# Optimization experiments

Measured on AMD Instinct MI355X. Metric: run time of the kernel, lower is better.

## Reference

```python
import jax, jax.numpy as jnp
import numpy as np

EMBED_SIZE = 1024
HEADS = 16
HEAD_DIM = EMBED_SIZE // HEADS  # 64


def setup_inputs() -> dict:
    key = jax.random.key(0)
    k_x, k_q, k_k, k_v, k_o, k_b = jax.random.split(key, 6)
    B, S = 32, 8192  # S divisible by HEADS
    x = jax.random.normal(k_x, (B, S, HEAD_DIM), dtype=jnp.float32)
    # torch.nn.Linear weights are [out, in]; scale ~ 1/sqrt(fan_in)
    s_h = 1.0 / np.sqrt(HEAD_DIM)
    s_e = 1.0 / np.sqrt(EMBED_SIZE)
    Wq = jax.random.uniform(k_q, (HEAD_DIM, HEAD_DIM), jnp.float32, -s_h, s_h)
    Wk = jax.random.uniform(k_k, (HEAD_DIM, HEAD_DIM), jnp.float32, -s_h, s_h)
    Wv = jax.random.uniform(k_v, (HEAD_DIM, HEAD_DIM), jnp.float32, -s_h, s_h)
    Wo = jax.random.uniform(k_o, (EMBED_SIZE, EMBED_SIZE), jnp.float32, -s_e, s_e)
    bo = jax.random.uniform(k_b, (EMBED_SIZE,), jnp.float32, -s_e, s_e)
    return {"x": x, "Wq": Wq, "Wk": Wk, "Wv": Wv, "Wo": Wo, "bo": bo}


def reference(x, Wq, Wk, Wv, Wo, bo):
    B = x.shape[0]
    # Q/K/V projections: Linear(head_dim, head_dim), bias=False -> x @ W.T
    Q = (x @ Wq.T).reshape(B, -1, HEADS, HEAD_DIM)  # [B, G, H, D], G = S/H
    K = (x @ Wk.T).reshape(B, -1, HEADS, HEAD_DIM)
    V = (x @ Wv.T).reshape(B, -1, HEADS, HEAD_DIM)
    # energy = Q @ K^T over last two dims -> [B, G, H, H]
    energy = jnp.einsum('bghd,bgkd->bghk', Q, K)
    attn = jax.nn.softmax(energy / jnp.sqrt(jnp.float32(EMBED_SIZE)), axis=3)
    out = jnp.einsum('bghk,bgkd->bghd', attn, V)      # [B, G, H, D]
    out = out.transpose(0, 2, 1, 3).reshape(B, -1, EMBED_SIZE)  # [B, S/H, E]
    return out @ Wo.T + bo
```

## Files before the change

### kernel.cpp

```cpp
#include <hip/hip_runtime.h>
#include <hip/hip_bf16.h>
#include <stdint.h>

#define TOKS   262144
#define NGRP   16384
#define EMB    1024
#define HD     64

using bf16x8 = __attribute__((ext_vector_type(8))) short;
using f32x4  = __attribute__((ext_vector_type(4))) float;

__device__ __forceinline__ unsigned pack2(float a, float b) {
    union { __hip_bfloat162 h; unsigned u; } cvt;
    cvt.h = __float22bfloat162_rn(make_float2(a, b));
    return cvt.u;
}
__device__ __forceinline__ bf16x8 cvt8(float4 v0, float4 v1) {
    uint4 u;
    u.x = pack2(v0.x, v0.y);
    u.y = pack2(v0.z, v0.w);
    u.z = pack2(v1.x, v1.y);
    u.w = pack2(v1.z, v1.w);
    return __builtin_bit_cast(bf16x8, u);
}
__device__ __forceinline__ void gload_lds16(const unsigned short* g, unsigned short* l) {
    __builtin_amdgcn_global_load_lds(
        (const __attribute__((address_space(1))) void*)g,
        (__attribute__((address_space(3))) void*)l,
        16, 0, 0);
}

__global__ __launch_bounds__(256) void k_cvt(const float* __restrict__ wo,
                                             const float* __restrict__ wq,
                                             const float* __restrict__ wk,
                                             const float* __restrict__ wv,
                                             unsigned short* __restrict__ wob,
                                             unsigned short* __restrict__ wqkvb) {
    int bid = blockIdx.x;
    if (bid < 512) {
        int tid = bid * 256 + threadIdx.x;
        int c   = tid >> 12;
        int nb  = (tid >> 6) & 63;
        int l   = tid & 63;
        int n   = nb * 16 + (l & 15);
        int k   = c * 32 + (l >> 4) * 8;
        const float* src = wo + (size_t)n * 1024 + k;
        float4 v0 = *(const float4*)(src);
        float4 v1 = *(const float4*)(src + 4);
        *(bf16x8*)(wob + (size_t)tid * 8) = cvt8(v0, v1);
    } else {
        int b = bid - 512;
        int m = b >> 2;
        const float* src = (m == 0) ? wq : ((m == 1) ? wk : wv);
        int idx = ((b & 3) * 256 + threadIdx.x) * 4;
        float4 v = *(const float4*)(src + idx);
        uint2 p;
        p.x = pack2(v.x, v.y);
        p.y = pack2(v.z, v.w);
        *(uint2*)(wqkvb + m * 4096 + idx) = p;
    }
}

#define SCL 0.0450842200278f

__global__ __launch_bounds__(256) void k_fused(const float* __restrict__ x,
                                               const unsigned short* __restrict__ wqkv,
                                               unsigned short* __restrict__ out2) {
    __shared__ __align__(16) unsigned short qkls[4][2][2][16 * 72];
    int t = threadIdx.x;
    int w = t >> 6, l = t & 63;
    int c = l & 15, q = l >> 4;
    int waveTok0 = blockIdx.x * 128 + w * 32;

    bf16x8 xa[2][2];
    #pragma unroll
    for (int g = 0; g < 2; ++g) {
        const float* xp = x + (size_t)(waveTok0 + g * 16 + c) * 64 + q * 8;
        #pragma unroll
        for (int kc = 0; kc < 2; ++kc) {
            float4 v0 = *(const float4*)(xp + kc * 32);
            float4 v1 = *(const float4*)(xp + kc * 32 + 4);
            xa[g][kc] = cvt8(v0, v1);
        }
    }

    uint2 pkV[2][4];
    #pragma unroll
    for (int m = 0; m < 3; ++m) {
        #pragma unroll
        for (int nb = 0; nb < 4; ++nb) {
            const unsigned short* wp = wqkv + m * 4096 + (nb * 16 + c) * 64 + q * 8;
            bf16x8 w0 = *(const bf16x8*)(wp);
            bf16x8 w1 = *(const bf16x8*)(wp + 32);
            #pragma unroll
            for (int g = 0; g < 2; ++g) {
                f32x4 acc = (f32x4){0.f, 0.f, 0.f, 0.f};
                acc = __builtin_amdgcn_mfma_f32_16x16x32_bf16(xa[g][0], w0, acc, 0, 0, 0);
                acc = __builtin_amdgcn_mfma_f32_16x16x32_bf16(xa[g][1], w1, acc, 0, 0, 0);
                unsigned u01 = pack2(acc[0], acc[1]);
                unsigned u23 = pack2(acc[2], acc[3]);
                if (m < 2) {
                    unsigned short* tile = qkls[w][g][m];
                    int base = 4 * q * 72 + nb * 16 + c;
                    tile[base]       = (unsigned short)u01;
                    tile[base + 72]  = (unsigned short)(u01 >> 16);
                    tile[base + 144] = (unsigned short)u23;
                    tile[base + 216] = (unsigned short)(u23 >> 16);
                } else {
                    pkV[g][nb].x = u01;
                    pkV[g][nb].y = u23;
                }
            }
        }
    }

    f32x4 e[2];
    #pragma unroll
    for (int g = 0; g < 2; ++g) {
        const unsigned short* Qt = qkls[w][g][0];
        const unsigned short* Kt = qkls[w][g][1];
        e[g] = (f32x4){0.f, 0.f, 0.f, 0.f};
        #pragma unroll
        for (int kc = 0; kc < 2; ++kc) {
            bf16x8 ka = *(const bf16x8*)(Kt + c * 72 + kc * 32 + q * 8);
            bf16x8 qb = *(const bf16x8*)(Qt + c * 72 + kc * 32 + q * 8);
            e[g] = __builtin_amdgcn_mfma_f32_16x16x32_bf16(ka, qb, e[g], 0, 0, 0);
        }
    }

    unsigned pa0[2], pa1[2];
    #pragma unroll
    for (int g = 0; g < 2; ++g) {
        float mx = fmaxf(fmaxf(e[g][0], e[g][1]), fmaxf(e[g][2], e[g][3]));
        mx = fmaxf(mx, __shfl_xor(mx, 16));
        mx = fmaxf(mx, __shfl_xor(mx, 32));
        float p0 = exp2f((e[g][0] - mx) * SCL);
        float p1 = exp2f((e[g][1] - mx) * SCL);
        float p2 = exp2f((e[g][2] - mx) * SCL);
        float p3 = exp2f((e[g][3] - mx) * SCL);
        float s = p0 + p1 + p2 + p3;
        s += __shfl_xor(s, 16);
        s += __shfl_xor(s, 32);
        float rinv = 1.0f / s;
        pa0[g] = pack2(p0 * rinv, p1 * rinv);
        pa1[g] = pack2(p2 * rinv, p3 * rinv);
    }

    int s0 = (32 * q + c) & 63;
    int s1 = (32 * q + 16 + c) & 63;
    int v0 = 32 * (q & 1) + c;
    int v1 = v0 + 16;
    bool hi = (q >= 2);
    #pragma unroll
    for (int g = 0; g < 2; ++g) {
        int a0 = __shfl((int)pa0[g], s0);
        int a1 = __shfl((int)pa1[g], s0);
        int a2 = __shfl((int)pa0[g], s1);
        int a3 = __shfl((int)pa1[g], s1);
        uint4 A2u;
        A2u.x = hi ? 0u : (unsigned)a0;
        A2u.y = hi ? 0u : (unsigned)a1;
        A2u.z = hi ? 0u : (unsigned)a2;
        A2u.w = hi ? 0u : (unsigned)a3;
        bf16x8 A2 = __builtin_bit_cast(bf16x8, A2u);

        unsigned short* Ot = qkls[w][g][0];
        #pragma unroll
        for (int nb = 0; nb < 4; ++nb) {
            uint4 B2u;
            B2u.x = (unsigned)__shfl((int)pkV[g][nb].x, v0);
            B2u.y = (unsigned)__shfl((int)pkV[g][nb].y, v0);
            B2u.z = (unsigned)__shfl((int)pkV[g][nb].x, v1);
            B2u.w = (unsigned)__shfl((int)pkV[g][nb].y, v1);
            bf16x8 B2 = __builtin_bit_cast(bf16x8, B2u);
            f32x4 o = (f32x4){0.f, 0.f, 0.f, 0.f};
            o = __builtin_amdgcn_mfma_f32_16x16x32_bf16(A2, B2, o, 0, 0, 0);
            unsigned u01 = pack2(o[0], o[1]);
            unsigned u23 = pack2(o[2], o[3]);
            int base = 4 * q * 72 + nb * 16 + c;
            Ot[base]       = (unsigned short)u01;
            Ot[base + 72]  = (unsigned short)(u01 >> 16);
            Ot[base + 144] = (unsigned short)u23;
            Ot[base + 216] = (unsigned short)(u23 >> 16);
        }
    }

    #pragma unroll
    for (int g = 0; g < 2; ++g) {
        int gi = (waveTok0 >> 4) + g;
        int b    = gi >> 9;
        int grem = gi & 511;
        int rowbase = b * 512 + (grem >> 4);
        int colpref = (grem & 15) * 64;
        const unsigned short* osrc = qkls[w][g][0] + (l >> 2) * 72 + (l & 3) * 16;
        uint4 ov0 = *(const uint4*)(osrc);
        uint4 ov1 = *(const uint4*)(osrc + 8);
        unsigned short* dst = out2 + (size_t)(rowbase + (l >> 2) * 32) * 1024
                                   + colpref + (l & 3) * 16;
        *(uint4*)(dst)     = ov0;
        *(uint4*)(dst + 8) = ov1;
    }
}

#define STG(gb, lb, half, kt) do { \
    gload_lds16((gb) + (size_t)(half) * 131072 + (size_t)(kt) * 64 + ga0, \
                (lb) + (half) * 8192 + lo0); \
    gload_lds16((gb) + (size_t)(half) * 131072 + (size_t)(kt) * 64 + ga1, \
                (lb) + (half) * 8192 + lo1); \
} while (0)

#define LDA4(buf, mh) do { \
    _Pragma("unroll") \
    for (int i2 = 0; i2 < 4; ++i2) { \
        const unsigned short* _p = (buf) + (wrow + ((mh) * 4 + i2) * 16 + lm) * 64; \
        a[i2][0] = *(const bf16x8*)(_p + jo0); \
        a[i2][1] = *(const bf16x8*)(_p + jo1); \
    } \
} while (0)

#define GLBB(d0, d1, gp) do { \
    _Pragma("unroll") \
    for (int kc = 0; kc < 2; ++kc) { \
        _Pragma("unroll") \
        for (int j2 = 0; j2 < 2; ++j2) { \
            d0[j2][kc] = *(const bf16x8*)((gp) + kc * 32768 + j2 * 512); \
            d1[j2][kc] = *(const bf16x8*)((gp) + kc * 32768 + (2 + j2) * 512); \
        } \
    } \
} while (0)

#define MM8(mh, nh, B) do { \
    _Pragma("unroll") \
    for (int i2 = 0; i2 < 4; ++i2) { \
        _Pragma("unroll") \
        for (int j2 = 0; j2 < 2; ++j2) { \
            acc[(mh)*4+i2][(nh)*2+j2] = __builtin_amdgcn_mfma_f32_16x16x32_bf16( \
                a[i2][0], B[j2][0], acc[(mh)*4+i2][(nh)*2+j2], 0, 0, 0); \
            acc[(mh)*4+i2][(nh)*2+j2] = __builtin_amdgcn_mfma_f32_16x16x32_bf16( \
                a[i2][1], B[j2][1], acc[(mh)*4+i2][(nh)*2+j2], 0, 0, 0); \
        } \
    } \
} while (0)

#define PHASE_MID() do { \
    __builtin_amdgcn_s_barrier(); \
    asm volatile("s_waitcnt lgkmcnt(0)" ::: "memory"); \
    __builtin_amdgcn_sched_barrier(0); \
    __builtin_amdgcn_s_setprio(1); \
} while (0)

#define PHASE_END() do { \
    __builtin_amdgcn_s_setprio(0); \
    __builtin_amdgcn_s_barrier(); \
} while (0)

#define TILE(t, c0, c1, n0_, n1_) do { \
    const int _t = (t); \
     \
    LDA4(pAr, 0); \
    if (_t < 15) GLBB(n0_, n1_, gB); \
    PHASE_MID(); MM8(0, 0, c0); PHASE_END(); \
     \
    if (_t < 14) STG(Ab, pAs, 0, _t + 2); \
    PHASE_MID(); MM8(0, 1, c1); PHASE_END(); \
     \
    LDA4(pAr, 1); \
    if (_t < 14) STG(Ab, pAs, 1, _t + 2); \
    PHASE_MID(); MM8(1, 1, c1); PHASE_END(); \
     \
    PHASE_MID(); MM8(1, 0, c0); \
    __builtin_amdgcn_s_setprio(0); \
    if (_t < 14)       { asm volatile("s_waitcnt vmcnt(4)" ::: "memory"); } \
    else if (_t == 14) { asm volatile("s_waitcnt vmcnt(0)" ::: "memory"); } \
    __builtin_amdgcn_s_barrier(); \
    unsigned short* _tmp = pAr; pAr = pAn; pAn = pAs; pAs = _tmp; \
    gB += 65536; \
} while (0)

__global__ __launch_bounds__(512, 2) void k_gemm256(const unsigned short* __restrict__ A,
                                                    const unsigned short* __restrict__ Bp,
                                                    const float* __restrict__ bias,
                                                    float* __restrict__ C) {
    extern __shared__ __align__(16) unsigned short lds[];
    unsigned short* As0 = lds;
    unsigned short* As1 = lds + 16384;
    unsigned short* As2 = lds + 32768;

    const int t = threadIdx.x;
    const int w = t >> 6, l = t & 63;
    const int lm = l & 15, q4 = l >> 4;
    const int jxor = lm & 7;
    const int jo0 = ((0 + q4) ^ jxor) * 8;
    const int jo1 = ((4 + q4) ^ jxor) * 8;

    const int bid = blockIdx.x;
    const int wg  = (bid & 7) * 32 + (bid >> 3);
    const int m0  = (wg >> 2) * 256;
    const int n0  = (wg & 3) * 256;

    const int wrow = (w >> 2) * 128;
    const int wcol = (w & 3) * 64;

    const int s1 = w * 128 + l;
    const int s2 = s1 + 64;
    const int r0 = s1 >> 3, c0 = s1 & 7;
    const int r1 = s2 >> 3, c1 = s2 & 7;
    const size_t ga0 = (size_t)r0 * 1024 + (size_t)((c0 ^ (r0 & 7)) * 8);
    const size_t ga1 = (size_t)r1 * 1024 + (size_t)((c1 ^ (r1 & 7)) * 8);
    const int lo0 = s1 * 8;
    const int lo1 = s2 * 8;

    const unsigned short* Ab = A + (size_t)m0 * 1024;
    const unsigned short* gB = Bp + (size_t)((n0 >> 4) + (wcol >> 4)) * 512
                                  + (size_t)l * 8;

    f32x4 acc[8][4];
    #pragma unroll
    for (int mi = 0; mi < 8; ++mi)
        #pragma unroll
        for (int ni = 0; ni < 4; ++ni)
            acc[mi][ni] = (f32x4){0.f, 0.f, 0.f, 0.f};

    unsigned short* pAr = As0;
    unsigned short* pAn = As1;
    unsigned short* pAs = As2;

    bf16x8 a[4][2];
    bf16x8 bE0[2][2], bE1[2][2], bO0[2][2], bO1[2][2];

    GLBB(bE0, bE1, gB);
    STG(Ab, pAr, 0, 0); STG(Ab, pAr, 1, 0);
    STG(Ab, pAn, 0, 1); STG(Ab, pAn, 1, 1);
    asm volatile("s_waitcnt vmcnt(4)" ::: "memory");
    __builtin_amdgcn_s_barrier();
    gB += 65536;

    #pragma unroll 1
    for (int tt = 0; tt < 8; ++tt) {
        TILE(2 * tt,     bE0, bE1, bO0, bO1);
        TILE(2 * tt + 1, bO0, bO1, bE0, bE1);
    }

    float bc[4];
    #pragma unroll
    for (int ni = 0; ni < 4; ++ni) bc[ni] = bias[n0 + wcol + ni * 16 + lm];
    #pragma unroll
    for (int mi = 0; mi < 8; ++mi) {
        #pragma unroll
        for (int r = 0; r < 4; ++r) {
            const int row = m0 + wrow + mi * 16 + q4 * 4 + r;
            float* cp = C + (size_t)row * 1024 + n0 + wcol + lm;
            #pragma unroll
            for (int ni = 0; ni < 4; ++ni)
                cp[ni * 16] = acc[mi][ni][r] + bc[ni];
        }
    }
}

extern "C" void kernel_launch(void* const* d_in, const int* in_sizes, int n_in,
                              void* d_out, int out_size, void* d_ws, size_t ws_size,
                              hipStream_t stream) {
    const float* x  = (const float*)d_in[0];
    const float* wq = (const float*)d_in[1];
    const float* wk = (const float*)d_in[2];
    const float* wv = (const float*)d_in[3];
    const float* wo = (const float*)d_in[4];
    const float* bo = (const float*)d_in[5];
    float* out = (float*)d_out;

    unsigned short* out2  = (unsigned short*)d_ws;
    unsigned short* wob   = out2 + (size_t)NGRP * 1024;
    unsigned short* wqkvb = wob + (size_t)EMB * EMB;

    static int s_once = []() {
        hipFuncSetAttribute((const void*)k_gemm256,
                            hipFuncAttributeMaxDynamicSharedMemorySize, 98304);
        return 0;
    }();
    (void)s_once;

    k_cvt    <<<524,  256, 0, stream>>>(wo, wq, wk, wv, wob, wqkvb);
    k_fused  <<<2048, 256, 0, stream>>>(x, wqkvb, out2);
    k_gemm256<<<256, 512, 98304, stream>>>(out2, wob, bo, out);
}
```

Before: 177.8 us.

## Fold weight conversion into fused attention kernel and restructure GEMM tile phases

Removes the separate weight-conversion kernel: the first 512 blocks of the fused attention kernel now also convert Wo to bf16, and every block converts the Wq/Wk/Wv fp32 rows to bf16 on the fly. This saves one kernel launch and the serialization between launches. In exchange, each block reads fp32 QKV weights redundantly, and the first 512 blocks take on extra work. The GEMM main loop is also restructured from four barrier-separated 8-MFMA phases into two 16-MFMA halves with fewer barriers, issuing the B register loads and A LDS staging up front.

Result: slower. 195.2 us (+9.8%).

```diff
diff --git a/kernel.cpp b/kernel.cpp
--- a/kernel.cpp
+++ b/kernel.cpp
@@ -30,15 +30,17 @@
         16, 0, 0);
 }
 
-__global__ __launch_bounds__(256) void k_cvt(const float* __restrict__ wo,
-                                             const float* __restrict__ wq,
-                                             const float* __restrict__ wk,
-                                             const float* __restrict__ wv,
-                                             unsigned short* __restrict__ wob,
-                                             unsigned short* __restrict__ wqkvb) {
-    int bid = blockIdx.x;
-    if (bid < 512) {
-        int tid = bid * 256 + threadIdx.x;
+#define SCL 0.0450842200278f
+
+__global__ __launch_bounds__(256) void k_fused(const float* __restrict__ x,
+                                               const float* __restrict__ wq,
+                                               const float* __restrict__ wk,
+                                               const float* __restrict__ wv,
+                                               const float* __restrict__ wo,
+                                               unsigned short* __restrict__ wob,
+                                               unsigned short* __restrict__ out2) {
+    if (blockIdx.x < 512) {
+        int tid = blockIdx.x * 256 + threadIdx.x;
         int c   = tid >> 12;
         int nb  = (tid >> 6) & 63;
         int l   = tid & 63;
@@ -48,24 +50,8 @@
         float4 v0 = *(const float4*)(src);
         float4 v1 = *(const float4*)(src + 4);
         *(bf16x8*)(wob + (size_t)tid * 8) = cvt8(v0, v1);
-    } else {
-        int b = bid - 512;
-        int m = b >> 2;
-        const float* src = (m == 0) ? wq : ((m == 1) ? wk : wv);
-        int idx = ((b & 3) * 256 + threadIdx.x) * 4;
-        float4 v = *(const float4*)(src + idx);
-        uint2 p;
-        p.x = pack2(v.x, v.y);
-        p.y = pack2(v.z, v.w);
-        *(uint2*)(wqkvb + m * 4096 + idx) = p;
-    }
-}
-
-#define SCL 0.0450842200278f
-
-__global__ __launch_bounds__(256) void k_fused(const float* __restrict__ x,
-                                               const unsigned short* __restrict__ wqkv,
-                                               unsigned short* __restrict__ out2) {
+    }
+
     __shared__ __align__(16) unsigned short qkls[4][2][2][16 * 72];
     int t = threadIdx.x;
     int w = t >> 6, l = t & 63;
@@ -87,11 +73,12 @@
     uint2 pkV[2][4];
     #pragma unroll
     for (int m = 0; m < 3; ++m) {
+        const float* Wsrc = (m == 0) ? wq : ((m == 1) ? wk : wv);
         #pragma unroll
         for (int nb = 0; nb < 4; ++nb) {
-            const unsigned short* wp = wqkv + m * 4096 + (nb * 16 + c) * 64 + q * 8;
-            bf16x8 w0 = *(const bf16x8*)(wp);
-            bf16x8 w1 = *(const bf16x8*)(wp + 32);
+            const float* wp = Wsrc + (size_t)(nb * 16 + c) * 64 + q * 8;
+            bf16x8 w0 = cvt8(*(const float4*)(wp),      *(const float4*)(wp + 4));
+            bf16x8 w1 = cvt8(*(const float4*)(wp + 32), *(const float4*)(wp + 36));
             #pragma unroll
             for (int g = 0; g < 2; ++g) {
                 f32x4 acc = (f32x4){0.f, 0.f, 0.f, 0.f};
@@ -218,62 +205,46 @@
     } \
 } while (0)
 
-#define GLBB(d0, d1, gp) do { \
+#define GLBB(d, gp) do { \
     _Pragma("unroll") \
-    for (int kc = 0; kc < 2; ++kc) { \
-        _Pragma("unroll") \
-        for (int j2 = 0; j2 < 2; ++j2) { \
-            d0[j2][kc] = *(const bf16x8*)((gp) + kc * 32768 + j2 * 512); \
-            d1[j2][kc] = *(const bf16x8*)((gp) + kc * 32768 + (2 + j2) * 512); \
-        } \
+    for (int n = 0; n < 4; ++n) { \
+        d[n][0] = *(const bf16x8*)((gp) + n * 512); \
+        d[n][1] = *(const bf16x8*)((gp) + 32768 + n * 512); \
     } \
 } while (0)
 
-#define MM8(mh, nh, B) do { \
+#define MM16(mh, B) do { \
     _Pragma("unroll") \
     for (int i2 = 0; i2 < 4; ++i2) { \
         _Pragma("unroll") \
-        for (int j2 = 0; j2 < 2; ++j2) { \
-            acc[(mh)*4+i2][(nh)*2+j2] = __builtin_amdgcn_mfma_f32_16x16x32_bf16( \
-                a[i2][0], B[j2][0], acc[(mh)*4+i2][(nh)*2+j2], 0, 0, 0); \
-            acc[(mh)*4+i2][(nh)*2+j2] = __builtin_amdgcn_mfma_f32_16x16x32_bf16( \
-                a[i2][1], B[j2][1], acc[(mh)*4+i2][(nh)*2+j2], 0, 0, 0); \
+        for (int n = 0; n < 4; ++n) { \
+            acc[(mh)*4+i2][n] = __builtin_amdgcn_mfma_f32_16x16x32_bf16( \
+                a[i2][0], B[n][0], acc[(mh)*4+i2][n], 0, 0, 0); \
+            acc[(mh)*4+i2][n] = __builtin_amdgcn_mfma_f32_16x16x32_bf16( \
+                a[i2][1], B[n][1], acc[(mh)*4+i2][n], 0, 0, 0); \
         } \
     } \
 } while (0)
 
-#define PHASE_MID() do { \
-    __builtin_amdgcn_s_barrier(); \
+#define TILE(_t, cB, nB) do { \
+    if ((_t) < 15) GLBB(nB, gB); \
+    if ((_t) < 14) { STG(Ab, pAs, 0, (_t) + 2); STG(Ab, pAs, 1, (_t) + 2); } \
+    LDA4(pAr, 0); \
     asm volatile("s_waitcnt lgkmcnt(0)" ::: "memory"); \
     __builtin_amdgcn_sched_barrier(0); \
     __builtin_amdgcn_s_setprio(1); \
-} while (0)
-
-#define PHASE_END() do { \
+    MM16(0, cB); \
     __builtin_amdgcn_s_setprio(0); \
+    LDA4(pAr, 1); \
+    asm volatile("s_waitcnt lgkmcnt(0)" ::: "memory"); \
+    __builtin_amdgcn_sched_barrier(0); \
+    __builtin_amdgcn_s_setprio(1); \
+    MM16(1, cB); \
+    __builtin_amdgcn_s_setprio(0); \
+    if ((_t) < 14)       { asm volatile("s_waitcnt vmcnt(4)" ::: "memory"); } \
+    else if ((_t) == 14) { asm volatile("s_waitcnt vmcnt(0)" ::: "memory"); } \
     __builtin_amdgcn_s_barrier(); \
-} while (0)
-
-#define TILE(t, c0, c1, n0_, n1_) do { \
-    const int _t = (t); \
-     \
-    LDA4(pAr, 0); \
-    if (_t < 15) GLBB(n0_, n1_, gB); \
-    PHASE_MID(); MM8(0, 0, c0); PHASE_END(); \
-     \
-    if (_t < 14) STG(Ab, pAs, 0, _t + 2); \
-    PHASE_MID(); MM8(0, 1, c1); PHASE_END(); \
-     \
-    LDA4(pAr, 1); \
-    if (_t < 14) STG(Ab, pAs, 1, _t + 2); \
-    PHASE_MID(); MM8(1, 1, c1); PHASE_END(); \
-     \
-    PHASE_MID(); MM8(1, 0, c0); \
-    __builtin_amdgcn_s_setprio(0); \
-    if (_t < 14)       { asm volatile("s_waitcnt vmcnt(4)" ::: "memory"); } \
-    else if (_t == 14) { asm volatile("s_waitcnt vmcnt(0)" ::: "memory"); } \
-    __builtin_amdgcn_s_barrier(); \
-    unsigned short* _tmp = pAr; pAr = pAn; pAn = pAs; pAs = _tmp; \
+    { unsigned short* _tmp = pAr; pAr = pAn; pAn = pAs; pAs = _tmp; } \
     gB += 65536; \
 } while (0)
 
@@ -326,9 +297,9 @@
     unsigned short* pAs = As2;
 
     bf16x8 a[4][2];
-    bf16x8 bE0[2][2], bE1[2][2], bO0[2][2], bO1[2][2];
-
-    GLBB(bE0, bE1, gB);
+    bf16x8 bC[4][2], bN[4][2];
+
+    GLBB(bC, gB);
     STG(Ab, pAr, 0, 0); STG(Ab, pAr, 1, 0);
     STG(Ab, pAn, 0, 1); STG(Ab, pAn, 1, 1);
     asm volatile("s_waitcnt vmcnt(4)" ::: "memory");
@@ -337,8 +308,8 @@
 
     #pragma unroll 1
     for (int tt = 0; tt < 8; ++tt) {
-        TILE(2 * tt,     bE0, bE1, bO0, bO1);
-        TILE(2 * tt + 1, bO0, bO1, bE0, bE1);
+        TILE(2 * tt,     bC, bN);
+        TILE(2 * tt + 1, bN, bC);
     }
 
     float bc[4];
@@ -368,9 +339,8 @@
     const float* bo = (const float*)d_in[5];
     float* out = (float*)d_out;
 
-    unsigned short* out2  = (unsigned short*)d_ws;
-    unsigned short* wob   = out2 + (size_t)NGRP * 1024;
-    unsigned short* wqkvb = wob + (size_t)EMB * EMB;
+    unsigned short* out2 = (unsigned short*)d_ws;
+    unsigned short* wob  = out2 + (size_t)NGRP * 1024;
 
     static int s_once = []() {
         hipFuncSetAttribute((const void*)k_gemm256,
@@ -379,7 +349,6 @@
     }();
     (void)s_once;
 
-    k_cvt    <<<524,  256, 0, stream>>>(wo, wq, wk, wv, wob, wqkvb);
-    k_fused  <<<2048, 256, 0, stream>>>(x, wqkvb, out2);
+    k_fused  <<<2048, 256, 0, stream>>>(x, wq, wk, wv, wo, wob, out2);
     k_gemm256<<<256, 512, 98304, stream>>>(out2, wob, bo, out);
 }
```
